# Performance work log

Measured on AMD Instinct MI355X. Metric: run time of the kernel, lower is better.

Reference implementation:

```python
import jax, jax.numpy as jnp
import numpy as np

N = 40000      # nodes
E = 640000     # edges (avg degree 16)
IN = 128       # in_dim
H = 8          # n_heads
D = 16         # out_dim per head
ED = 64        # edge_dim
C = H * D      # out_channel = 128 == IN -> residual is Identity
EPS = 1e-5


def setup_inputs() -> dict:
    key = jax.random.key(0)
    ks = jax.random.split(key, 20)

    def lin(k, shape):
        fan_in = shape[-1]
        return jax.random.normal(k, shape, dtype=jnp.float32) / np.sqrt(fan_in)

    return {
        "q": jax.random.normal(ks[0], (N, IN), dtype=jnp.float32),
        "k": jax.random.normal(ks[1], (N, IN), dtype=jnp.float32),
        "v": jax.random.normal(ks[2], (N, IN), dtype=jnp.float32),
        "edge_feat": jax.random.normal(ks[3], (E, ED), dtype=jnp.float32),
        "src": jax.random.randint(ks[4], (E,), 0, N, dtype=jnp.int32),
        "dst": jax.random.randint(ks[5], (E,), 0, N, dtype=jnp.int32),
        "Wq": lin(ks[6], (C, IN)),
        "Wk": lin(ks[7], (C, IN)),
        "Wv": lin(ks[8], (C, IN)),
        "We": lin(ks[9], (H, ED)),
        "be": jnp.zeros((H,), dtype=jnp.float32),
        "Wo": lin(ks[10], (C, C)),
        "W1": lin(ks[11], (2 * C, C)),
        "b1": jnp.zeros((2 * C,), dtype=jnp.float32),
        "W2": lin(ks[12], (C, 2 * C)),
        "b2": jnp.zeros((C,), dtype=jnp.float32),
        "g1": jnp.ones((C,), dtype=jnp.float32),
        "bt1": jnp.zeros((C,), dtype=jnp.float32),
        "g2": jnp.ones((C,), dtype=jnp.float32),
        "bt2": jnp.zeros((C,), dtype=jnp.float32),
    }


def _batch_norm(x, g, b):
    mu = x.mean(axis=0)
    var = x.var(axis=0)  # biased, matching torch BN normalization
    return (x - mu) * jax.lax.rsqrt(var + EPS) * g + b


def reference(q, k, v, edge_feat, src, dst, Wq, Wk, Wv, We, be, Wo,
              W1, b1, W2, b2, g1, bt1, g2, bt2):
    n = q.shape[0]
    qd = (q @ Wq.T).reshape(n, H, D)        # [N,H,D] dst queries
    ksrc = (k @ Wk.T).reshape(-1, H, D)     # [N,H,D]
    vsrc = (v @ Wv.T).reshape(-1, H, D)     # [N,H,D]

    # per-edge attention scores: v_dot_u(q_dst, k_src) / sqrt(D)
    scores = jnp.einsum('ehd,ehd->eh', qd[dst], ksrc[src]) / jnp.sqrt(jnp.float32(D))
    # edge_mode == 'ADD': add per-head edge bias
    scores = scores + edge_feat @ We.T + be  # [E,H]

    # edge softmax normalized by destination node (segment softmax)
    smax = jax.ops.segment_max(scores, dst, num_segments=n)      # [N,H]
    ex = jnp.exp(scores - smax[dst])
    denom = jax.ops.segment_sum(ex, dst, num_segments=n)         # [N,H]
    attn = ex / denom[dst]                                       # [E,H]

    # scatter-weighted aggregation: sum_e attn * v_src -> dst
    agg = jax.ops.segment_sum(attn[:, :, None] * vsrc[src], dst, num_segments=n)  # [N,H,D]

    rst = agg.reshape(n, C) @ Wo.T
    rst = rst + q                    # residual (Identity: in_dim == out_channel)
    rst = _batch_norm(rst, g1, bt1)

    h = jnp.maximum(rst @ W1.T + b1, 0.0) @ W2.T + b2  # FFN
    rst = _batch_norm(h + rst, g2, bt2)
    return rst
```

## Files before the change

kernel.cpp:

```cpp
#include <hip/hip_runtime.h>
#include <cstdint>
#include <cstddef>

#define Nn 40000
#define Ne 640000
#define CC 128
#define EPSbn 1e-5f

typedef __attribute__((ext_vector_type(8))) __bf16 bf16x8;
typedef __attribute__((ext_vector_type(4))) float floatx4;

__device__ inline unsigned short f2bf(float x){
  union { float f; unsigned u; } c; c.f = x;
  unsigned r = c.u + 0x7fffu + ((c.u >> 16) & 1u);
  return (unsigned short)(r >> 16);
}
__device__ inline float bflo(unsigned u){ return __uint_as_float(u << 16); }
__device__ inline float bfhi(unsigned u){ return __uint_as_float(u & 0xffff0000u); }

__global__ void zero_k(int* __restrict__ p, int n){
  int i = blockIdx.x*blockDim.x + threadIdx.x;
  if (i < n) p[i] = 0;
}

struct GA3 {
  const void* A0; const void* A1; const void* A2;
  const float* W0; const float* W1; const float* W2;
  void* C0; void* C1; void* C2;
  int m0, m1, m2;
};

template<int KTILES,bool ABF16,bool HASBIAS,bool HASRES,bool RELU,bool AFFA,bool AFFRES,bool BNSTAT>
__global__ __launch_bounds__(256,2) void mgemm_k(
    GA3 ga, const float* __restrict__ bias, const float* __restrict__ res,
    const float* __restrict__ sc, const float* __restrict__ sh,
    float* __restrict__ bnS, float* __restrict__ bnQ,
    int M, int Ncols)
{
  constexpr int K = KTILES * 128;
  __shared__ __align__(16) unsigned short As[128*136];
  __shared__ __align__(16) unsigned short Ws[128*136];
  const int z = blockIdx.z;
  const void*  Ap = (z==0) ? ga.A0 : (z==1) ? ga.A1 : ga.A2;
  const float* W  = (z==0) ? ga.W0 : (z==1) ? ga.W1 : ga.W2;
  void*        Cp = (z==0) ? ga.C0 : (z==1) ? ga.C1 : ga.C2;
  const int mode  = (z==0) ? ga.m0 : (z==1) ? ga.m1 : ga.m2;

  const int tid  = threadIdx.x;
  const int lane = tid & 63;
  const int wv   = tid >> 6;
  const int m    = lane & 15;
  const int quad = lane >> 4;
  const int row0 = blockIdx.x * 128;
  const int col0 = blockIdx.y * 128;
  floatx4 acc[2][8] = {};

  for (int kt = 0; kt < K; kt += 128) {
    #pragma unroll 4
    for (int it = 0; it < 16; ++it) {
      int s = tid + it*256;
      int r = s >> 5;
      int c = (s & 31) << 2;
      int gr = row0 + r; if (gr >= M) gr = M - 1;
      ushort4 ua;
      if (ABF16) {
        ua = *(const ushort4*)((const unsigned short*)Ap + (size_t)gr*K + kt + c);
      } else {
        float4 a4 = *(const float4*)((const float*)Ap + (size_t)gr*K + kt + c);
        if (AFFA) {
          int kk = kt + c;
          a4.x = a4.x*sc[kk  ] + sh[kk  ];
          a4.y = a4.y*sc[kk+1] + sh[kk+1];
          a4.z = a4.z*sc[kk+2] + sh[kk+2];
          a4.w = a4.w*sc[kk+3] + sh[kk+3];
        }
        ua.x = f2bf(a4.x); ua.y = f2bf(a4.y); ua.z = f2bf(a4.z); ua.w = f2bf(a4.w);
      }
      *(ushort4*)&As[r*136 + c] = ua;
      float4 w4 = *(const float4*)(W + (size_t)(col0 + r)*K + kt + c);
      ushort4 uw;
      uw.x = f2bf(w4.x); uw.y = f2bf(w4.y); uw.z = f2bf(w4.z); uw.w = f2bf(w4.w);
      *(ushort4*)&Ws[r*136 + c] = uw;
    }
    __syncthreads();
    #pragma unroll
    for (int ks = 0; ks < 4; ++ks) {
      int ko = ks*32 + quad*8;
      bf16x8 a0 = *(const bf16x8*)&As[(32*wv      + m)*136 + ko];
      bf16x8 a1 = *(const bf16x8*)&As[(32*wv + 16 + m)*136 + ko];
      #pragma unroll
      for (int j = 0; j < 8; ++j) {
        bf16x8 bj = *(const bf16x8*)&Ws[(16*j + m)*136 + ko];
        acc[0][j] = __builtin_amdgcn_mfma_f32_16x16x32_bf16(a0, bj, acc[0][j], 0, 0, 0);
        acc[1][j] = __builtin_amdgcn_mfma_f32_16x16x32_bf16(a1, bj, acc[1][j], 0, 0, 0);
      }
    }
    __syncthreads();
  }

  float bcol[8], scv[8], shv[8];
  #pragma unroll
  for (int j = 0; j < 8; ++j) {
    int gcol = col0 + 16*j + m;
    if (HASBIAS) bcol[j] = bias[gcol];
    if (AFFRES) { scv[j] = sc[gcol]; shv[j] = sh[gcol]; }
  }
  float ps[8] = {}, pq[8] = {};
  #pragma unroll
  for (int rt = 0; rt < 2; ++rt) {
    #pragma unroll
    for (int rg = 0; rg < 4; ++rg) {
      int grow = row0 + 32*wv + 16*rt + quad*4 + rg;
      if (grow < M) {
        #pragma unroll
        for (int j = 0; j < 8; ++j) {
          int gcol = col0 + 16*j + m;
          float o = acc[rt][j][rg];
          if (HASBIAS) o += bcol[j];
          if (HASRES) {
            float rr = res[(size_t)grow*Ncols + gcol];
            if (AFFRES) rr = rr*scv[j] + shv[j];
            o += rr;
          }
          if (RELU) o = fmaxf(o, 0.f);
          if (BNSTAT) { ps[j] += o; pq[j] += o*o; }
          if (mode == 0)      ((float*)Cp)[(size_t)grow*Ncols + gcol] = o;
          else if (mode == 1) ((unsigned short*)Cp)[(size_t)grow*Ncols + gcol] = f2bf(o);
          else {
            int ph = mode - 2;
            *(unsigned short*)((char*)Cp + (size_t)grow*512 + (gcol>>1)*8 + ph*4 + (gcol&1)*2) = f2bf(o);
          }
        }
      }
    }
  }
  if (BNSTAT) {
    float* sS = (float*)&As[0];
    float* sQ = sS + 4*128;
    #pragma unroll
    for (int j = 0; j < 8; ++j) {
      float s = ps[j], qq = pq[j];
      s += __shfl_xor(s, 16); qq += __shfl_xor(qq, 16);
      s += __shfl_xor(s, 32); qq += __shfl_xor(qq, 32);
      if (quad == 0) { sS[wv*128 + 16*j + m] = s; sQ[wv*128 + 16*j + m] = qq; }
    }
    __syncthreads();
    if (wv == 0) {
      #pragma unroll
      for (int c = 0; c < 128; c += 64) {
        int cc = c + lane;
        float s  = sS[cc] + sS[128+cc] + sS[256+cc] + sS[384+cc];
        float qq = sQ[cc] + sQ[128+cc] + sQ[256+cc] + sQ[384+cc];
        atomicAdd(&bnS[col0 + cc], s);
        atomicAdd(&bnQ[col0 + cc], qq);
      }
    }
  }
}

__global__ __launch_bounds__(256) void ebias_k(
    const float* __restrict__ ef, const float* __restrict__ We,
    const float* __restrict__ be, const int* __restrict__ pos,
    unsigned short* __restrict__ EBs)
{
  __shared__ float efs[32][68];
  __shared__ float Wes[8][68];
  __shared__ float bes[8];
  int tid = threadIdx.x;
  if (tid < 8) bes[tid] = be[tid];
  for (int i = tid; i < 512; i += 256) Wes[i>>6][i&63] = We[i];
  int e0 = blockIdx.x * 32;
  #pragma unroll
  for (int l = 0; l < 2; ++l) {
    int idx = tid + l*256;
    int r   = idx >> 4;
    int q4  = (idx & 15) << 2;
    float4 t = *(const float4*)(ef + (size_t)(e0 + r)*64 + q4);
    efs[r][q4]=t.x; efs[r][q4+1]=t.y; efs[r][q4+2]=t.z; efs[r][q4+3]=t.w;
  }
  __syncthreads();
  int h = tid & 7, el = tid >> 3;
  int e = e0 + el;
  float es = 0.f;
  #pragma unroll
  for (int kk = 0; kk < 64; kk += 4) {
    float4 a = *(const float4*)&efs[el][kk];
    float4 b = *(const float4*)&Wes[h][kk];
    es += a.x*b.x + a.y*b.y + a.z*b.z + a.w*b.w;
  }
  EBs[(size_t)pos[e]*8 + h] = f2bf(es + bes[h]);
}

__global__ void hist_k(const int* __restrict__ dst, int* __restrict__ counts, int E){
  int i = blockIdx.x*blockDim.x + threadIdx.x;
  if (i < E) atomicAdd(&counts[dst[i]], 1);
}

__global__ __launch_bounds__(256) void scan1_k(
    const int* __restrict__ counts, int* __restrict__ part,
    int* __restrict__ bsums, int n)
{
  int tid = threadIdx.x;
  int base = blockIdx.x*1024 + tid*4;
  int v0 = (base   < n) ? counts[base  ] : 0;
  int v1 = (base+1 < n) ? counts[base+1] : 0;
  int v2 = (base+2 < n) ? counts[base+2] : 0;
  int v3 = (base+3 < n) ? counts[base+3] : 0;
  int t1 = v0+v1, t2 = t1+v2, t3 = t2+v3;
  int lane = tid & 63, wv = tid >> 6;
  int x = t3;
  #pragma unroll
  for (int off = 1; off < 64; off <<= 1) {
    int y = __shfl_up(x, off);
    if (lane >= off) x += y;
  }
  __shared__ int wt[4];
  if (lane == 63) wt[wv] = x;
  __syncthreads();
  int wbase = 0;
  #pragma unroll
  for (int w = 0; w < 4; ++w) if (w < wv) wbase += wt[w];
  int excl = wbase + x - t3;
  if (base   < n) part[base  ] = excl;
  if (base+1 < n) part[base+1] = excl + v0;
  if (base+2 < n) part[base+2] = excl + t1;
  if (base+3 < n) part[base+3] = excl + t2;
  if (tid == 255) bsums[blockIdx.x] = wbase + x;
}

__global__ void scan2_k(int* bsums, int nb){
  int lane = threadIdx.x;
  int v = (lane < nb) ? bsums[lane] : 0;
  int x = v;
  #pragma unroll
  for (int off = 1; off < 64; off <<= 1) {
    int y = __shfl_up(x, off);
    if (lane >= off) x += y;
  }
  if (lane < nb) bsums[lane] = x - v;
}

__global__ void scan3_k(int* __restrict__ offsets, const int* __restrict__ bsums,
                        int* __restrict__ cursor, int n, int E){
  int i = blockIdx.x*blockDim.x + threadIdx.x;
  if (i < n) {
    int o = offsets[i] + bsums[i >> 10];
    offsets[i] = o;
    cursor[i]  = o;
  }
  if (i == 0) offsets[n] = E;
}

__global__ void scatter_k(const int* __restrict__ dst, const int* __restrict__ src,
                          int* __restrict__ cursor, int* __restrict__ pos,
                          int* __restrict__ srcs, int E){
  int i = blockIdx.x*blockDim.x + threadIdx.x;
  if (i < E) {
    int p = atomicAdd(&cursor[dst[i]], 1);
    pos[i]  = p;
    srcs[p] = src[i];
  }
}

__global__ __launch_bounds__(256) void agg_k(
    const unsigned* __restrict__ QDb, const uint2* __restrict__ KV,
    const unsigned short* __restrict__ EBs,
    const int* __restrict__ offsets, const int* __restrict__ srcs,
    float* __restrict__ agg, int n)
{
  int wv = threadIdx.x >> 6, lane = threadIdx.x & 63;
  int node = blockIdx.x*4 + wv;
  if (node >= n) return;
  unsigned qt = QDb[(size_t)node*64 + lane];
  float q0 = bflo(qt) * 0.25f;
  float q1 = bfhi(qt) * 0.25f;
  int beg = offsets[node], end = offsets[node+1];
  int hoff = lane >> 3;
  float acc0 = 0.f, acc1 = 0.f, den = 0.f;
  for (int base = beg; base < end; base += 64) {
    int mrem = end - base; if (mrem > 64) mrem = 64;
    int ss = (lane < mrem) ? srcs[base + lane] : 0;
    int j = 0;
    for (; j + 4 <= mrem; j += 4) {
      int s0 = __shfl(ss, j);
      int s1 = __shfl(ss, j+1);
      int s2 = __shfl(ss, j+2);
      int s3 = __shfl(ss, j+3);
      uint2 kv0 = KV[(size_t)s0*64 + lane];
      uint2 kv1 = KV[(size_t)s1*64 + lane];
      uint2 kv2 = KV[(size_t)s2*64 + lane];
      uint2 kv3 = KV[(size_t)s3*64 + lane];
      float p0 = q0*bflo(kv0.x) + q1*bfhi(kv0.x);
      float p1 = q0*bflo(kv1.x) + q1*bfhi(kv1.x);
      float p2 = q0*bflo(kv2.x) + q1*bfhi(kv2.x);
      float p3 = q0*bflo(kv3.x) + q1*bfhi(kv3.x);
      p0 += __shfl_xor(p0, 1); p1 += __shfl_xor(p1, 1); p2 += __shfl_xor(p2, 1); p3 += __shfl_xor(p3, 1);
      p0 += __shfl_xor(p0, 2); p1 += __shfl_xor(p1, 2); p2 += __shfl_xor(p2, 2); p3 += __shfl_xor(p3, 2);
      p0 += __shfl_xor(p0, 4); p1 += __shfl_xor(p1, 4); p2 += __shfl_xor(p2, 4); p3 += __shfl_xor(p3, 4);
      float eb0 = __uint_as_float(((unsigned)EBs[(size_t)(base+j  )*8 + hoff]) << 16);
      float eb1 = __uint_as_float(((unsigned)EBs[(size_t)(base+j+1)*8 + hoff]) << 16);
      float eb2 = __uint_as_float(((unsigned)EBs[(size_t)(base+j+2)*8 + hoff]) << 16);
      float eb3 = __uint_as_float(((unsigned)EBs[(size_t)(base+j+3)*8 + hoff]) << 16);
      float w0 = __expf(p0 + eb0);
      float w1 = __expf(p1 + eb1);
      float w2 = __expf(p2 + eb2);
      float w3 = __expf(p3 + eb3);
      acc0 += w0*bflo(kv0.y) + w1*bflo(kv1.y) + w2*bflo(kv2.y) + w3*bflo(kv3.y);
      acc1 += w0*bfhi(kv0.y) + w1*bfhi(kv1.y) + w2*bfhi(kv2.y) + w3*bfhi(kv3.y);
      den  += (w0 + w1) + (w2 + w3);
    }
    for (; j < mrem; ++j) {
      int s0 = __shfl(ss, j);
      uint2 kv0 = KV[(size_t)s0*64 + lane];
      float p0 = q0*bflo(kv0.x) + q1*bfhi(kv0.x);
      p0 += __shfl_xor(p0, 1);
      p0 += __shfl_xor(p0, 2);
      p0 += __shfl_xor(p0, 4);
      float eb0 = __uint_as_float(((unsigned)EBs[(size_t)(base+j)*8 + hoff]) << 16);
      float w0 = __expf(p0 + eb0);
      acc0 += w0*bflo(kv0.y);
      acc1 += w0*bfhi(kv0.y);
      den  += w0;
    }
  }
  float inv = den > 0.f ? 1.f/den : 0.f;
  float2 o; o.x = acc0*inv; o.y = acc1*inv;
  *(float2*)(agg + (size_t)node*128 + 2*lane) = o;
}

__global__ void bnfin_k(const float* sum, const float* sq, const float* g,
                        const float* bt, float* scale, float* shift, int M){
  int c = threadIdx.x;
  float mu  = sum[c] / (float)M;
  float var = sq[c] / (float)M - mu*mu;
  float s = g[c] * rsqrtf(var + EPSbn);
  scale[c] = s;
  shift[c] = bt[c] - mu*s;
}

__global__ void bnapply_k(const float* __restrict__ Y, const float* __restrict__ scale,
                          const float* __restrict__ shift, float* __restrict__ out, int total){
  int n4 = total >> 2;
  for (int i = blockIdx.x*blockDim.x + threadIdx.x; i < n4; i += gridDim.x*blockDim.x) {
    float4 vv = ((const float4*)Y)[i];
    int c = (i << 2) & 127;
    vv.x = vv.x*scale[c  ] + shift[c  ];
    vv.y = vv.y*scale[c+1] + shift[c+1];
    vv.z = vv.z*scale[c+2] + shift[c+2];
    vv.w = vv.w*scale[c+3] + shift[c+3];
    ((float4*)out)[i] = vv;
  }
}

extern "C" void kernel_launch(void* const* d_in, const int* in_sizes, int n_in,
                              void* d_out, int out_size, void* d_ws, size_t ws_size,
                              hipStream_t stream) {
  const float* q   = (const float*)d_in[0];
  const float* k   = (const float*)d_in[1];
  const float* v   = (const float*)d_in[2];
  const float* ef  = (const float*)d_in[3];
  const int*   src = (const int*)d_in[4];
  const int*   dst = (const int*)d_in[5];
  const float* Wq  = (const float*)d_in[6];
  const float* Wk  = (const float*)d_in[7];
  const float* Wv  = (const float*)d_in[8];
  const float* We  = (const float*)d_in[9];
  const float* be  = (const float*)d_in[10];
  const float* Wo  = (const float*)d_in[11];
  const float* W1  = (const float*)d_in[12];
  const float* b1  = (const float*)d_in[13];
  const float* W2  = (const float*)d_in[14];
  const float* b2  = (const float*)d_in[15];
  const float* g1  = (const float*)d_in[16];
  const float* bt1 = (const float*)d_in[17];
  const float* g2  = (const float*)d_in[18];
  const float* bt2 = (const float*)d_in[19];
  float* out = (float*)d_out;

  float* ws = (float*)d_ws;
  const size_t NB = (size_t)Nn * CC;
  float* QDb = ws;
  float* KV  = ws + NB/2;
  unsigned short* EBs = (unsigned short*)(ws + 3*NB/2);
  float* AGG = ws + 2*NB;
  float* RST = ws + 3*NB;
  float* H1  = ws;
  float* Y   = AGG;
  float* bn = ws + 4*NB;
  float* sum1 = bn;       float* sq1 = bn+128;  float* sc1 = bn+256; float* sh1 = bn+384;
  float* sum2 = bn+512;   float* sq2 = bn+640;  float* sc2 = bn+768; float* sh2 = bn+896;
  int* ib      = (int*)(bn + 1024);
  int* counts  = ib;
  int* offsets = ib + 40000;
  int* cursor  = ib + 80001;
  int* posA    = ib + 120001;
  int* srcsA   = ib + 760001;
  int* bsums   = ib + 1400001;

  zero_k<<<dim3(161), 256, 0, stream>>>((int*)bn, 1024 + Nn);

  hist_k<<<dim3(2500), 256, 0, stream>>>(dst, counts, Ne);
  scan1_k<<<dim3(40), 256, 0, stream>>>(counts, offsets, bsums, Nn);
  scan2_k<<<dim3(1), 64, 0, stream>>>(bsums, 40);
  scan3_k<<<dim3(157), 256, 0, stream>>>(offsets, bsums, cursor, Nn, Ne);
  scatter_k<<<dim3(2500), 256, 0, stream>>>(dst, src, cursor, posA, srcsA, Ne);

  {
    GA3 ga;
    ga.A0 = q;  ga.A1 = k;  ga.A2 = v;
    ga.W0 = Wq; ga.W1 = Wk; ga.W2 = Wv;
    ga.C0 = QDb; ga.C1 = KV; ga.C2 = KV;
    ga.m0 = 1; ga.m1 = 2; ga.m2 = 3;
    mgemm_k<1,false,false,false,false,false,false,false><<<dim3(313,1,3),256,0,stream>>>(
        ga, nullptr, nullptr, nullptr, nullptr, nullptr, nullptr, Nn, 128);
  }

  ebias_k<<<dim3(Ne/32), 256, 0, stream>>>(ef, We, be, posA, EBs);

  agg_k<<<dim3(Nn/4), 256, 0, stream>>>((const unsigned*)QDb, (const uint2*)KV, EBs,
                                        offsets, srcsA, AGG, Nn);

  {
    GA3 ga = {};
    ga.A0 = AGG; ga.W0 = Wo; ga.C0 = RST; ga.m0 = 0;
    mgemm_k<1,false,false,true,false,false,false,true><<<dim3(313,1,1),256,0,stream>>>(
        ga, nullptr, q, nullptr, nullptr, sum1, sq1, Nn, 128);
  }
  bnfin_k<<<dim3(1), 128, 0, stream>>>(sum1, sq1, g1, bt1, sc1, sh1, Nn);

  {
    GA3 ga = {};
    ga.A0 = RST; ga.W0 = W1; ga.C0 = H1; ga.m0 = 1;
    mgemm_k<1,false,true,false,true,true,false,false><<<dim3(313,2,1),256,0,stream>>>(
        ga, b1, nullptr, sc1, sh1, nullptr, nullptr, Nn, 256);
  }

  {
    GA3 ga = {};
    ga.A0 = H1; ga.W0 = W2; ga.C0 = Y; ga.m0 = 0;
    mgemm_k<2,true,true,true,false,false,true,true><<<dim3(313,1,1),256,0,stream>>>(
        ga, b2, RST, sc1, sh1, sum2, sq2, Nn, 128);
  }
  bnfin_k<<<dim3(1), 128, 0, stream>>>(sum2, sq2, g2, bt2, sc2, sh2, Nn);
  bnapply_k<<<dim3(1024), 256, 0, stream>>>(Y, sc2, sh2, out, Nn*CC);
}
```

Measured before the change: 574.3 us.

## Store K and V in FP8 E4M3 to halve gather traffic in aggregation

The projection GEMM now writes K and V as plain bf16 arrays. A new repack kernel converts them to FP8 E4M3 and interleaves them into one 32-bit word per lane. The aggregation kernel gathers 4 bytes per lane per edge instead of 8 and decodes with the hardware fp8 conversion when available. This targets the random-gather bandwidth of the edge loop, at the cost of an extra pass over K/V and a large loss of precision in the attention scores and values.

```diff
diff --git a/kernel.cpp b/kernel.cpp
--- a/kernel.cpp
+++ b/kernel.cpp
@@ -17,6 +17,42 @@
 }
 __device__ inline float bflo(unsigned u){ return __uint_as_float(u << 16); }
 __device__ inline float bfhi(unsigned u){ return __uint_as_float(u & 0xffff0000u); }
+
+__device__ inline unsigned f2e4m3(float x){
+  unsigned u = __float_as_uint(x);
+  unsigned s = (u >> 24) & 0x80u;
+  unsigned a = u & 0x7fffffffu;
+  unsigned lsb = (a >> 20) & 1u;
+  a += 0x0007FFFFu + lsb;
+  int e = (int)((a >> 23) & 0xffu) - 127;
+  unsigned b;
+  if (e < -9)      b = 0u;
+  else if (e < -6) b = (unsigned)(int)rintf(__uint_as_float(u & 0x7fffffffu) * 512.f);
+  else if (e > 8)  b = 0x7Eu;
+  else             b = (unsigned)(((e + 7) << 3) | ((a >> 20) & 7u));
+  if ((b & 0x7fu) == 0x7fu) b = 0x7Eu;
+  return s | b;
+}
+
+#if defined(__has_builtin)
+#if __has_builtin(__builtin_amdgcn_cvt_f32_fp8)
+#define FP8_HW 1
+#endif
+#endif
+template<int SEL>
+__device__ inline float fp8dec(unsigned w){
+#ifdef FP8_HW
+  return __builtin_amdgcn_cvt_f32_fp8((int)w, SEL);
+#else
+  unsigned b = (w >> (SEL*8)) & 0xffu;
+  unsigned s = (b & 0x80u) << 24;
+  unsigned em = b & 0x7fu;
+  float v;
+  if (em >= 8) v = __uint_as_float((((em >> 3) + 117u) << 23)) * (float)(8 + (em & 7));
+  else         v = (float)em * 0.001953125f;
+  return __uint_as_float(__float_as_uint(v) | s);
+#endif
+}
 
 __global__ void zero_k(int* __restrict__ p, int n){
   int i = blockIdx.x*blockDim.x + threadIdx.x;
@@ -124,12 +160,8 @@
           }
           if (RELU) o = fmaxf(o, 0.f);
           if (BNSTAT) { ps[j] += o; pq[j] += o*o; }
-          if (mode == 0)      ((float*)Cp)[(size_t)grow*Ncols + gcol] = o;
-          else if (mode == 1) ((unsigned short*)Cp)[(size_t)grow*Ncols + gcol] = f2bf(o);
-          else {
-            int ph = mode - 2;
-            *(unsigned short*)((char*)Cp + (size_t)grow*512 + (gcol>>1)*8 + ph*4 + (gcol&1)*2) = f2bf(o);
-          }
+          if (mode == 0) ((float*)Cp)[(size_t)grow*Ncols + gcol] = o;
+          else           ((unsigned short*)Cp)[(size_t)grow*Ncols + gcol] = f2bf(o);
         }
       }
     }
@@ -155,6 +187,20 @@
         atomicAdd(&bnQ[col0 + cc], qq);
       }
     }
+  }
+}
+
+__global__ __launch_bounds__(256) void repack_k(
+    const unsigned* __restrict__ Kb, const unsigned* __restrict__ Vb,
+    unsigned* __restrict__ KV, int total)
+{
+  int i = blockIdx.x*blockDim.x + threadIdx.x;
+  if (i < total) {
+    unsigned kk = Kb[i];
+    unsigned vv = Vb[i];
+    unsigned o = f2e4m3(bflo(kk)) | (f2e4m3(bfhi(kk)) << 8)
+               | (f2e4m3(bflo(vv)) << 16) | (f2e4m3(bfhi(vv)) << 24);
+    KV[i] = o;
   }
 }
 
@@ -263,7 +309,7 @@
 }
 
 __global__ __launch_bounds__(256) void agg_k(
-    const unsigned* __restrict__ QDb, const uint2* __restrict__ KV,
+    const unsigned* __restrict__ QDb, const unsigned* __restrict__ KV,
     const unsigned short* __restrict__ EBs,
     const int* __restrict__ offsets, const int* __restrict__ srcs,
     float* __restrict__ agg, int n)
@@ -286,14 +332,14 @@
       int s1 = __shfl(ss, j+1);
       int s2 = __shfl(ss, j+2);
       int s3 = __shfl(ss, j+3);
-      uint2 kv0 = KV[(size_t)s0*64 + lane];
-      uint2 kv1 = KV[(size_t)s1*64 + lane];
-      uint2 kv2 = KV[(size_t)s2*64 + lane];
-      uint2 kv3 = KV[(size_t)s3*64 + lane];
-      float p0 = q0*bflo(kv0.x) + q1*bfhi(kv0.x);
-      float p1 = q0*bflo(kv1.x) + q1*bfhi(kv1.x);
-      float p2 = q0*bflo(kv2.x) + q1*bfhi(kv2.x);
-      float p3 = q0*bflo(kv3.x) + q1*bfhi(kv3.x);
+      unsigned kv0 = KV[(size_t)s0*64 + lane];
+      unsigned kv1 = KV[(size_t)s1*64 + lane];
+      unsigned kv2 = KV[(size_t)s2*64 + lane];
+      unsigned kv3 = KV[(size_t)s3*64 + lane];
+      float p0 = q0*fp8dec<0>(kv0) + q1*fp8dec<1>(kv0);
+      float p1 = q0*fp8dec<0>(kv1) + q1*fp8dec<1>(kv1);
+      float p2 = q0*fp8dec<0>(kv2) + q1*fp8dec<1>(kv2);
+      float p3 = q0*fp8dec<0>(kv3) + q1*fp8dec<1>(kv3);
       p0 += __shfl_xor(p0, 1); p1 += __shfl_xor(p1, 1); p2 += __shfl_xor(p2, 1); p3 += __shfl_xor(p3, 1);
       p0 += __shfl_xor(p0, 2); p1 += __shfl_xor(p1, 2); p2 += __shfl_xor(p2, 2); p3 += __shfl_xor(p3, 2);
       p0 += __shfl_xor(p0, 4); p1 += __shfl_xor(p1, 4); p2 += __shfl_xor(p2, 4); p3 += __shfl_xor(p3, 4);
@@ -305,21 +351,21 @@
       float w1 = __expf(p1 + eb1);
       float w2 = __expf(p2 + eb2);
       float w3 = __expf(p3 + eb3);
-      acc0 += w0*bflo(kv0.y) + w1*bflo(kv1.y) + w2*bflo(kv2.y) + w3*bflo(kv3.y);
-      acc1 += w0*bfhi(kv0.y) + w1*bfhi(kv1.y) + w2*bfhi(kv2.y) + w3*bfhi(kv3.y);
+      acc0 += w0*fp8dec<2>(kv0) + w1*fp8dec<2>(kv1) + w2*fp8dec<2>(kv2) + w3*fp8dec<2>(kv3);
+      acc1 += w0*fp8dec<3>(kv0) + w1*fp8dec<3>(kv1) + w2*fp8dec<3>(kv2) + w3*fp8dec<3>(kv3);
       den  += (w0 + w1) + (w2 + w3);
     }
     for (; j < mrem; ++j) {
       int s0 = __shfl(ss, j);
-      uint2 kv0 = KV[(size_t)s0*64 + lane];
-      float p0 = q0*bflo(kv0.x) + q1*bfhi(kv0.x);
+      unsigned kv0 = KV[(size_t)s0*64 + lane];
+      float p0 = q0*fp8dec<0>(kv0) + q1*fp8dec<1>(kv0);
       p0 += __shfl_xor(p0, 1);
       p0 += __shfl_xor(p0, 2);
       p0 += __shfl_xor(p0, 4);
       float eb0 = __uint_as_float(((unsigned)EBs[(size_t)(base+j)*8 + hoff]) << 16);
       float w0 = __expf(p0 + eb0);
-      acc0 += w0*bflo(kv0.y);
-      acc1 += w0*bfhi(kv0.y);
+      acc0 += w0*fp8dec<2>(kv0);
+      acc1 += w0*fp8dec<3>(kv0);
       den  += w0;
     }
   }
@@ -380,13 +426,15 @@
   float* ws = (float*)d_ws;
   const size_t NB = (size_t)Nn * CC;
   float* QDb = ws;
-  float* KV  = ws + NB/2;
-  unsigned short* EBs = (unsigned short*)(ws + 3*NB/2);
-  float* AGG = ws + 2*NB;
-  float* RST = ws + 3*NB;
+  float* Kb  = ws + NB/2;
+  float* Vb  = ws + NB;
+  unsigned* KVq = (unsigned*)(ws + 3*NB/2);
+  unsigned short* EBs = (unsigned short*)(ws + 2*NB);
+  float* AGG = ws + 5*NB/2;
+  float* RST = ws + 7*NB/2;
   float* H1  = ws;
   float* Y   = AGG;
-  float* bn = ws + 4*NB;
+  float* bn = ws + 9*NB/2;
   float* sum1 = bn;       float* sq1 = bn+128;  float* sc1 = bn+256; float* sh1 = bn+384;
   float* sum2 = bn+512;   float* sq2 = bn+640;  float* sc2 = bn+768; float* sh2 = bn+896;
   int* ib      = (int*)(bn + 1024);
@@ -409,15 +457,18 @@
     GA3 ga;
     ga.A0 = q;  ga.A1 = k;  ga.A2 = v;
     ga.W0 = Wq; ga.W1 = Wk; ga.W2 = Wv;
-    ga.C0 = QDb; ga.C1 = KV; ga.C2 = KV;
-    ga.m0 = 1; ga.m1 = 2; ga.m2 = 3;
+    ga.C0 = QDb; ga.C1 = Kb; ga.C2 = Vb;
+    ga.m0 = 1; ga.m1 = 1; ga.m2 = 1;
     mgemm_k<1,false,false,false,false,false,false,false><<<dim3(313,1,3),256,0,stream>>>(
         ga, nullptr, nullptr, nullptr, nullptr, nullptr, nullptr, Nn, 128);
   }
 
+  repack_k<<<dim3(10000), 256, 0, stream>>>((const unsigned*)Kb, (const unsigned*)Vb,
+                                            KVq, Nn*64);
+
   ebias_k<<<dim3(Ne/32), 256, 0, stream>>>(ef, We, be, posA, EBs);
 
-  agg_k<<<dim3(Nn/4), 256, 0, stream>>>((const unsigned*)QDb, (const uint2*)KV, EBs,
+  agg_k<<<dim3(Nn/4), 256, 0, stream>>>((const unsigned*)QDb, KVq, EBs,
                                         offsets, srcsA, AGG, Nn);
 
   {
```

Result: faster. 543.7 us (-5.3%).
